# Kernel tuning notes

Measured on AMD Instinct MI355X. Metric: run time of the kernel, lower is better.

The kernel has to match this reference:

```python
import jax, jax.numpy as jnp
import numpy as np

B, S, H = 32, 256, 128
K, C, DSUB, O = 8, 4096, 16, 6  # PQ subspaces, ncentroids=4096, subvector dim, bits/symbol


def setup_inputs() -> dict:
    key = jax.random.key(0)
    ks = jax.random.split(key, 8)
    return {
        "z": jax.random.normal(ks[0], (B, S, 3), jnp.float32),
        "W1": jax.random.normal(ks[1], (3, H), jnp.float32) * 0.3,
        "b1": jax.random.normal(ks[2], (H,), jnp.float32) * 0.1,
        "W2": jax.random.normal(ks[3], (H, H), jnp.float32) * 0.1,
        "b2": jax.random.normal(ks[4], (H,), jnp.float32) * 0.1,
        "centroids": jax.random.normal(ks[5], (K, C, DSUB), jnp.float32),
        "W3": jax.random.normal(ks[6], (H, O), jnp.float32) * 0.1,
        "b3": jax.random.normal(ks[7], (O,), jnp.float32) * 0.1,
    }


def reference(z, W1, b1, W2, b2, centroids, W3, b3):
    # Small demapper MLP (layers 1-2, exact dense math)
    h1 = jax.nn.relu(z @ W1 + b1)            # [B,S,H]
    h2 = jax.nn.relu(h1 @ W2 + b2)           # [B,S,H] == layer3in
    N = B * S
    x = h2.reshape(N, K, DSUB)               # split rows into K PQ subvectors
    # Encode: nearest centroid per subspace (||x-c||^2 argmin; ||x||^2 is constant per row)
    dots = jnp.einsum("nkd,kcd->nkc", x, centroids)      # [N,K,C]
    c_norm = jnp.sum(centroids * centroids, axis=-1)      # [K,C]
    codes = jnp.argmin(c_norm[None, :, :] - 2.0 * dots, axis=-1)  # [N,K] int
    # LUT: precomputed centroid @ W3 per subspace
    W3r = W3.reshape(K, DSUB, O)
    lut = jnp.einsum("kcd,kdo->kco", centroids, W3r)      # [K,C,O]
    # Approximate matmul: sum of LUT entries selected by codes
    approx = jnp.sum(lut[jnp.arange(K)[None, :], codes], axis=1)  # [N,O]
    llr = (approx + b3).reshape(B, S * O)                 # [B, n]
    return llr
```

## Files before the change

kernel.cpp:

```cpp
#include <hip/hip_runtime.h>
#include <stdint.h>

#define NROWS 8192
#define HDIM  128
#define KSUB  8
#define NC    4096
#define DSUB  16
#define OUTD  6


__global__ __launch_bounds__(256) void mlp_kernel(
    const float* __restrict__ z, const float* __restrict__ W1, const float* __restrict__ b1,
    const float* __restrict__ W2, const float* __restrict__ b2,
    const float* __restrict__ centroids,
    float* __restrict__ x, float* __restrict__ cnorm,
    unsigned long long* __restrict__ minpack)
{
    __shared__ float h1s[32 * HDIM];
    __shared__ float w2s[HDIM * HDIM];
    const int t = threadIdx.x;
    const int row0 = blockIdx.x * 32;

    minpack[blockIdx.x * 256 + t] = 0xFFFFFFFFFFFFFFFFull;

    if (blockIdx.x < (KSUB * NC) / 256) {
        const int g = blockIdx.x * 256 + t;
        const float4* cp = (const float4*)&centroids[(size_t)g * DSUB];
        float nn = 0.f;
        #pragma unroll
        for (int q = 0; q < 4; ++q) {
            const float4 v = cp[q];
            nn = fmaf(v.x, v.x, nn); nn = fmaf(v.y, v.y, nn);
            nn = fmaf(v.z, v.z, nn); nn = fmaf(v.w, v.w, nn);
        }
        cnorm[g] = nn;
    }

    {
        const float4* g4 = (const float4*)W2;
        float4* s4 = (float4*)w2s;
        #pragma unroll
        for (int q = 0; q < 16; ++q) s4[t + q * 256] = g4[t + q * 256];
    }

    #pragma unroll
    for (int e = 0; e < 16; ++e) {
        const int idx = e * 256 + t;
        const int r = idx >> 7, j = idx & 127;
        const int n = row0 + r;
        float acc = b1[j];
        acc = fmaf(z[n * 3 + 0], W1[0 * HDIM + j], acc);
        acc = fmaf(z[n * 3 + 1], W1[1 * HDIM + j], acc);
        acc = fmaf(z[n * 3 + 2], W1[2 * HDIM + j], acc);
        h1s[idx] = fmaxf(acc, 0.f);
    }
    __syncthreads();

    const int c4 = (t & 31) * 4;
    const int r4 = (t >> 5) * 4;
    float acc[4][4];
    #pragma unroll
    for (int a = 0; a < 4; ++a)
        #pragma unroll
        for (int b = 0; b < 4; ++b) acc[a][b] = 0.f;

    for (int k4 = 0; k4 < HDIM; k4 += 4) {
        float hh[4][4], ww[4][4];
        #pragma unroll
        for (int q = 0; q < 4; ++q) {
            const float4 v = *(const float4*)&h1s[(r4 + q) * HDIM + k4];
            hh[q][0] = v.x; hh[q][1] = v.y; hh[q][2] = v.z; hh[q][3] = v.w;
        }
        #pragma unroll
        for (int p = 0; p < 4; ++p) {
            const float4 v = *(const float4*)&w2s[(k4 + p) * HDIM + c4];
            ww[p][0] = v.x; ww[p][1] = v.y; ww[p][2] = v.z; ww[p][3] = v.w;
        }
        #pragma unroll
        for (int q = 0; q < 4; ++q)
            #pragma unroll
            for (int p = 0; p < 4; ++p) {
                acc[q][0] = fmaf(hh[q][p], ww[p][0], acc[q][0]);
                acc[q][1] = fmaf(hh[q][p], ww[p][1], acc[q][1]);
                acc[q][2] = fmaf(hh[q][p], ww[p][2], acc[q][2]);
                acc[q][3] = fmaf(hh[q][p], ww[p][3], acc[q][3]);
            }
    }

    const float4 bb = *(const float4*)&b2[c4];
    #pragma unroll
    for (int q = 0; q < 4; ++q) {
        float4 o;
        o.x = fmaxf(acc[q][0] + bb.x, 0.f);
        o.y = fmaxf(acc[q][1] + bb.y, 0.f);
        o.z = fmaxf(acc[q][2] + bb.z, 0.f);
        o.w = fmaxf(acc[q][3] + bb.w, 0.f);
        *(float4*)&x[(size_t)(row0 + r4 + q) * HDIM + c4] = o;
    }
}

#define RPT 4

__global__ __launch_bounds__(256) void argmin_kernel(
    const float* __restrict__ x, const float* __restrict__ centroids,
    const float* __restrict__ cnorm, unsigned long long* __restrict__ minpack)
{
    __shared__ float cs[256 * DSUB];
    __shared__ float cn[256];
    const int t = threadIdx.x;
    const int rb = blockIdx.x;
    const int k  = blockIdx.y;
    const int cz = blockIdx.z;
    const int row0 = rb * 1024 + t;
    const int cb = cz * 256;

    float xr[RPT][DSUB];
    #pragma unroll
    for (int rr = 0; rr < RPT; ++rr) {
        const float* xp = &x[(size_t)(row0 + rr * 256) * HDIM + k * DSUB];
        #pragma unroll
        for (int q = 0; q < DSUB; q += 4) {
            const float4 v = *(const float4*)&xp[q];
            xr[rr][q + 0] = v.x; xr[rr][q + 1] = v.y;
            xr[rr][q + 2] = v.z; xr[rr][q + 3] = v.w;
        }
    }

    {
        const float4* gp = (const float4*)&centroids[((size_t)k * NC + cb) * DSUB];
        float4* sp = (float4*)cs;
        #pragma unroll
        for (int q = 0; q < 4; ++q) sp[t + q * 256] = gp[t + q * 256];
        cn[t] = cnorm[k * NC + cb + t];
    }
    __syncthreads();

    float mv[RPT]; int mi[RPT];
    #pragma unroll
    for (int rr = 0; rr < RPT; ++rr) { mv[rr] = 1e30f; mi[rr] = 0; }

    for (int cc = 0; cc < 256; ++cc) {
        const float4 c0 = *(const float4*)&cs[cc * DSUB + 0];
        const float4 c1 = *(const float4*)&cs[cc * DSUB + 4];
        const float4 c2 = *(const float4*)&cs[cc * DSUB + 8];
        const float4 c3 = *(const float4*)&cs[cc * DSUB + 12];
        const float nrm = cn[cc];
        #pragma unroll
        for (int rr = 0; rr < RPT; ++rr) {
            float d;
            d = xr[rr][0] * c0.x;
            d = fmaf(xr[rr][1],  c0.y, d);
            d = fmaf(xr[rr][2],  c0.z, d);
            d = fmaf(xr[rr][3],  c0.w, d);
            d = fmaf(xr[rr][4],  c1.x, d);
            d = fmaf(xr[rr][5],  c1.y, d);
            d = fmaf(xr[rr][6],  c1.z, d);
            d = fmaf(xr[rr][7],  c1.w, d);
            d = fmaf(xr[rr][8],  c2.x, d);
            d = fmaf(xr[rr][9],  c2.y, d);
            d = fmaf(xr[rr][10], c2.z, d);
            d = fmaf(xr[rr][11], c2.w, d);
            d = fmaf(xr[rr][12], c3.x, d);
            d = fmaf(xr[rr][13], c3.y, d);
            d = fmaf(xr[rr][14], c3.z, d);
            d = fmaf(xr[rr][15], c3.w, d);
            const float s = fmaf(d, -2.f, nrm);
            if (s < mv[rr]) { mv[rr] = s; mi[rr] = cb + cc; }
        }
    }

    #pragma unroll
    for (int rr = 0; rr < RPT; ++rr) {
        unsigned u = __float_as_uint(mv[rr]);
        u = (u & 0x80000000u) ? ~u : (u | 0x80000000u);
        atomicMin(&minpack[(size_t)(row0 + rr * 256) * KSUB + k],
                  ((unsigned long long)u << 32) | (unsigned)mi[rr]);
    }
}

__global__ __launch_bounds__(256) void out_kernel(
    const float* __restrict__ centroids, const float* __restrict__ W3,
    const float* __restrict__ b3, const unsigned long long* __restrict__ minpack,
    float* __restrict__ out)
{
    const int gid = blockIdx.x * 256 + threadIdx.x;
    const int n = gid / OUTD;
    const int o = gid - n * OUTD;
    float acc = b3[o];
    #pragma unroll
    for (int k = 0; k < KSUB; ++k) {
        const int code = (int)(minpack[(size_t)n * KSUB + k] & 0xFFFFFFFFull);
        const float* cp = &centroids[((size_t)k * NC + code) * DSUB];
        const float* wp = &W3[(k * DSUB) * OUTD + o];
        #pragma unroll
        for (int d = 0; d < DSUB; ++d)
            acc = fmaf(cp[d], wp[d * OUTD], acc);
    }
    out[gid] = acc;
}

extern "C" void kernel_launch(void* const* d_in, const int* in_sizes, int n_in,
                              void* d_out, int out_size, void* d_ws, size_t ws_size,
                              hipStream_t stream)
{
    const float* z  = (const float*)d_in[0];
    const float* W1 = (const float*)d_in[1];
    const float* b1 = (const float*)d_in[2];
    const float* W2 = (const float*)d_in[3];
    const float* b2 = (const float*)d_in[4];
    const float* ce = (const float*)d_in[5];
    const float* W3 = (const float*)d_in[6];
    const float* b3 = (const float*)d_in[7];

    char* ws = (char*)d_ws;
    float* x = (float*)ws;
    unsigned long long* minpack = (unsigned long long*)(ws + (size_t)NROWS * HDIM * 4);
    float* cnorm = (float*)(ws + (size_t)NROWS * HDIM * 4 + (size_t)NROWS * KSUB * 8);

    hipLaunchKernelGGL(mlp_kernel, dim3(NROWS / 32), dim3(256), 0, stream,
                       z, W1, b1, W2, b2, ce, x, cnorm, minpack);
    hipLaunchKernelGGL(argmin_kernel, dim3(8, 8, 16), dim3(256), 0, stream,
                       x, ce, cnorm, minpack);
    hipLaunchKernelGGL(out_kernel, dim3((NROWS * OUTD) / 256), dim3(256), 0, stream,
                       ce, W3, b3, minpack, (float*)d_out);
}
```

Before: 200.6 us.

## Read centroids via uniform scalar loads and double rows per thread in argmin

The MLP output is stored subspace-major so each argmin thread reads a contiguous 16-float subvector. The argmin kernel drops its LDS centroid staging and barrier and reads centroids directly from global memory with wave-uniform addresses, which the compiler can turn into scalar loads. Rows per thread go from 4 to 8 and centroids per block from 256 to 128. The -2 factor is folded into x so the norm seeds the FMA chain. This raises register pressure and may change float rounding slightly, which can flip argmin ties.

```diff
diff --git a/kernel.cpp b/kernel.cpp
--- a/kernel.cpp
+++ b/kernel.cpp
@@ -13,7 +13,7 @@
     const float* __restrict__ z, const float* __restrict__ W1, const float* __restrict__ b1,
     const float* __restrict__ W2, const float* __restrict__ b2,
     const float* __restrict__ centroids,
-    float* __restrict__ x, float* __restrict__ cnorm,
+    float* __restrict__ xk, float* __restrict__ cnorm,
     unsigned long long* __restrict__ minpack)
 {
     __shared__ float h1s[32 * HDIM];
@@ -88,6 +88,8 @@
     }
 
     const float4 bb = *(const float4*)&b2[c4];
+    const int kk = c4 >> 4;
+    const int dd = c4 & 15;
     #pragma unroll
     for (int q = 0; q < 4; ++q) {
         float4 o;
@@ -95,76 +97,67 @@
         o.y = fmaxf(acc[q][1] + bb.y, 0.f);
         o.z = fmaxf(acc[q][2] + bb.z, 0.f);
         o.w = fmaxf(acc[q][3] + bb.w, 0.f);
-        *(float4*)&x[(size_t)(row0 + r4 + q) * HDIM + c4] = o;
-    }
-}
-
-#define RPT 4
+        *(float4*)&xk[((size_t)kk * NROWS + (row0 + r4 + q)) * DSUB + dd] = o;
+    }
+}
+
+#define RPT 8
+#define CPB 128
 
 __global__ __launch_bounds__(256) void argmin_kernel(
-    const float* __restrict__ x, const float* __restrict__ centroids,
+    const float* __restrict__ xk, const float* __restrict__ centroids,
     const float* __restrict__ cnorm, unsigned long long* __restrict__ minpack)
 {
-    __shared__ float cs[256 * DSUB];
-    __shared__ float cn[256];
     const int t = threadIdx.x;
     const int rb = blockIdx.x;
     const int k  = blockIdx.y;
     const int cz = blockIdx.z;
-    const int row0 = rb * 1024 + t;
-    const int cb = cz * 256;
+    const int row0 = rb * 2048 + t;
+    const int cb = cz * CPB;
 
     float xr[RPT][DSUB];
     #pragma unroll
     for (int rr = 0; rr < RPT; ++rr) {
-        const float* xp = &x[(size_t)(row0 + rr * 256) * HDIM + k * DSUB];
+        const float* xp = &xk[((size_t)k * NROWS + row0 + rr * 256) * DSUB];
         #pragma unroll
         for (int q = 0; q < DSUB; q += 4) {
             const float4 v = *(const float4*)&xp[q];
-            xr[rr][q + 0] = v.x; xr[rr][q + 1] = v.y;
-            xr[rr][q + 2] = v.z; xr[rr][q + 3] = v.w;
-        }
-    }
-
-    {
-        const float4* gp = (const float4*)&centroids[((size_t)k * NC + cb) * DSUB];
-        float4* sp = (float4*)cs;
-        #pragma unroll
-        for (int q = 0; q < 4; ++q) sp[t + q * 256] = gp[t + q * 256];
-        cn[t] = cnorm[k * NC + cb + t];
-    }
-    __syncthreads();
+            xr[rr][q + 0] = -2.f * v.x; xr[rr][q + 1] = -2.f * v.y;
+            xr[rr][q + 2] = -2.f * v.z; xr[rr][q + 3] = -2.f * v.w;
+        }
+    }
 
     float mv[RPT]; int mi[RPT];
     #pragma unroll
     for (int rr = 0; rr < RPT; ++rr) { mv[rr] = 1e30f; mi[rr] = 0; }
 
-    for (int cc = 0; cc < 256; ++cc) {
-        const float4 c0 = *(const float4*)&cs[cc * DSUB + 0];
-        const float4 c1 = *(const float4*)&cs[cc * DSUB + 4];
-        const float4 c2 = *(const float4*)&cs[cc * DSUB + 8];
-        const float4 c3 = *(const float4*)&cs[cc * DSUB + 12];
-        const float nrm = cn[cc];
+    const float* cp  = &centroids[((size_t)k * NC + cb) * DSUB];
+    const float* cnp = &cnorm[k * NC + cb];
+
+    #pragma unroll 2
+    for (int cc = 0; cc < CPB; ++cc) {
+        float c[DSUB];
+        #pragma unroll
+        for (int d = 0; d < DSUB; ++d) c[d] = cp[cc * DSUB + d];
+        const float nrm = cnp[cc];
         #pragma unroll
         for (int rr = 0; rr < RPT; ++rr) {
-            float d;
-            d = xr[rr][0] * c0.x;
-            d = fmaf(xr[rr][1],  c0.y, d);
-            d = fmaf(xr[rr][2],  c0.z, d);
-            d = fmaf(xr[rr][3],  c0.w, d);
-            d = fmaf(xr[rr][4],  c1.x, d);
-            d = fmaf(xr[rr][5],  c1.y, d);
-            d = fmaf(xr[rr][6],  c1.z, d);
-            d = fmaf(xr[rr][7],  c1.w, d);
-            d = fmaf(xr[rr][8],  c2.x, d);
-            d = fmaf(xr[rr][9],  c2.y, d);
-            d = fmaf(xr[rr][10], c2.z, d);
-            d = fmaf(xr[rr][11], c2.w, d);
-            d = fmaf(xr[rr][12], c3.x, d);
-            d = fmaf(xr[rr][13], c3.y, d);
-            d = fmaf(xr[rr][14], c3.z, d);
-            d = fmaf(xr[rr][15], c3.w, d);
-            const float s = fmaf(d, -2.f, nrm);
+            float s = fmaf(xr[rr][0], c[0], nrm);
+            s = fmaf(xr[rr][1],  c[1],  s);
+            s = fmaf(xr[rr][2],  c[2],  s);
+            s = fmaf(xr[rr][3],  c[3],  s);
+            s = fmaf(xr[rr][4],  c[4],  s);
+            s = fmaf(xr[rr][5],  c[5],  s);
+            s = fmaf(xr[rr][6],  c[6],  s);
+            s = fmaf(xr[rr][7],  c[7],  s);
+            s = fmaf(xr[rr][8],  c[8],  s);
+            s = fmaf(xr[rr][9],  c[9],  s);
+            s = fmaf(xr[rr][10], c[10], s);
+            s = fmaf(xr[rr][11], c[11], s);
+            s = fmaf(xr[rr][12], c[12], s);
+            s = fmaf(xr[rr][13], c[13], s);
+            s = fmaf(xr[rr][14], c[14], s);
+            s = fmaf(xr[rr][15], c[15], s);
             if (s < mv[rr]) { mv[rr] = s; mi[rr] = cb + cc; }
         }
     }
@@ -213,14 +206,14 @@
     const float* b3 = (const float*)d_in[7];
 
     char* ws = (char*)d_ws;
-    float* x = (float*)ws;
+    float* xk = (float*)ws;
     unsigned long long* minpack = (unsigned long long*)(ws + (size_t)NROWS * HDIM * 4);
     float* cnorm = (float*)(ws + (size_t)NROWS * HDIM * 4 + (size_t)NROWS * KSUB * 8);
 
     hipLaunchKernelGGL(mlp_kernel, dim3(NROWS / 32), dim3(256), 0, stream,
-                       z, W1, b1, W2, b2, ce, x, cnorm, minpack);
-    hipLaunchKernelGGL(argmin_kernel, dim3(8, 8, 16), dim3(256), 0, stream,
-                       x, ce, cnorm, minpack);
+                       z, W1, b1, W2, b2, ce, xk, cnorm, minpack);
+    hipLaunchKernelGGL(argmin_kernel, dim3(4, 8, 32), dim3(256), 0, stream,
+                       xk, ce, cnorm, minpack);
     hipLaunchKernelGGL(out_kernel, dim3((NROWS * OUTD) / 256), dim3(256), 0, stream,
                        ce, W3, b3, minpack, (float*)d_out);
 }
```

After: 256.7 us. +28.0%, slower.
